# Kernel tuning notes

Measured on AMD Instinct MI355X. Metric: run time of the kernel, lower is better.

The kernel has to match this reference:

```python
import jax, jax.numpy as jnp
import numpy as np

TWO_PI = 2.0 * np.pi


def _grid_sample(w, g):
    """Bilinear sample. w: [M,C,H,W]; g: [M,2,H,W] coords in [-1,1] (x,y),
    align_corners=True, border-clamped."""
    H, W = w.shape[-2], w.shape[-1]
    x = (g[:, 0] + 1.0) * 0.5 * (W - 1)  # [M,H,W]
    y = (g[:, 1] + 1.0) * 0.5 * (H - 1)
    x0 = jnp.floor(x)
    y0 = jnp.floor(y)
    fx = x - x0
    fy = y - y0
    x0i = jnp.clip(x0.astype(jnp.int32), 0, W - 1)
    x1i = jnp.clip(x0i + 1, 0, W - 1)
    y0i = jnp.clip(y0.astype(jnp.int32), 0, H - 1)
    y1i = jnp.clip(y0i + 1, 0, H - 1)

    def samp(wm, yi, xi):
        return wm[:, yi, xi]  # [C,H,W]

    v00 = jax.vmap(samp)(w, y0i, x0i)
    v01 = jax.vmap(samp)(w, y0i, x1i)
    v10 = jax.vmap(samp)(w, y1i, x0i)
    v11 = jax.vmap(samp)(w, y1i, x1i)
    fx = fx[:, None]  # broadcast over channel dim
    fy = fy[:, None]
    return (1 - fy) * ((1 - fx) * v00 + fx * v01) + fy * ((1 - fx) * v10 + fx * v11)


def _forward(in_H, out_H, weight, grid_H, grid_Rn, mask):
    No, Ni = out_H.shape[0], in_H.shape[0]
    N = grid_H.shape[0]
    Gk, Cout, Cin, kh, kw = weight.shape

    # inverse_H: angles negate; left_apply_to_H: angles add (pairwise)
    out_inv = -out_H  # [No,1]
    theta = (out_inv[:, None, 0] + in_H[None, :, 0]).reshape(-1)  # [No*Ni]

    # interpolate_H: periodic linear interp over uniform angle grid
    step = TWO_PI / N
    pos = jnp.mod(theta, TWO_PI) / step
    i0 = jnp.floor(pos).astype(jnp.int32) % N
    i1 = (i0 + 1) % N
    frac = (pos - jnp.floor(pos))[:, None]
    wflat = weight.reshape(Gk, -1)  # [Gk, Cout*Cin*kh*kw]
    w = (1.0 - frac) * wflat[i0] + frac * wflat[i1]  # [No*Ni, C]
    w = w.reshape(No * Ni, Cin * Cout, kh, kw)

    # left_apply_to_Rn: rotate spatial grid by out_H^{-1}
    ang = out_inv[:, 0]
    c, s = jnp.cos(ang), jnp.sin(ang)
    gx = c[:, None, None] * grid_Rn[0] - s[:, None, None] * grid_Rn[1]
    gy = s[:, None, None] * grid_Rn[0] + c[:, None, None] * grid_Rn[1]
    grids = jnp.stack([gx, gy], axis=1)  # [No,2,kh,kw]
    grids = jnp.repeat(grids, Ni, axis=0)  # repeat_interleave -> [No*Ni,2,kh,kw]

    # interpolate_Rn: bilinear grid sample
    w = _grid_sample(w, grids)  # [No*Ni, Cin*Cout, kh, kw]
    w = w.reshape(No, Ni, Cin, Cout, kh, kw)
    # .transpose(0,3).transpose(1,3) -> [Cout, No, Cin, Ni, kh, kw]
    w = jnp.transpose(w, (3, 0, 2, 1, 4, 5))
    return mask * w


def setup_inputs() -> dict:
    key = jax.random.key(0)
    k1, k2, k3 = jax.random.split(key, 3)
    N, Cout, Cin, ks = 8, 128, 128, 5
    in_H = jax.random.uniform(k1, (N, 1), dtype=jnp.float32) * TWO_PI
    out_H = jax.random.uniform(k2, (N, 1), dtype=jnp.float32) * TWO_PI
    fan_in = Cin * ks * ks
    weight = jax.random.normal(k3, (N, Cout, Cin, ks, ks), dtype=jnp.float32) / np.sqrt(fan_in)
    grid_H = (jnp.arange(N) * (TWO_PI / N)).astype(jnp.float32)
    lin = jnp.linspace(-1.0, 1.0, ks)
    X, Y = jnp.meshgrid(lin, lin, indexing='xy')
    grid_Rn = jnp.stack([X, Y]).astype(jnp.float32)  # [2, ks, ks]
    mask = (X ** 2 + Y ** 2 <= 1.0 + 1e-6).astype(jnp.float32)  # circular mask
    return dict(in_H=in_H, out_H=out_H, weight=weight, grid_H=grid_H,
                grid_Rn=grid_Rn, mask=mask)


def reference(in_H, out_H, weight, grid_H, grid_Rn, mask):
    return _forward(in_H, out_H, weight, grid_H, grid_Rn, mask)
```

## Files before the change

kernel.cpp:

```cpp
#include <hip/hip_runtime.h>
#include <math.h>


#define TWO_PI_F 6.28318530717958647692f
#define G_STRIDE 808

__global__ __launch_bounds__(256) void rotconv_weight_kernel(
    const float* __restrict__ in_H,
    const float* __restrict__ out_H,
    const float* __restrict__ weight,
    const float* __restrict__ grid_Rn,
    const float* __restrict__ mask,
    float* __restrict__ out)
{
    __shared__ __align__(16) float s_w[8 * G_STRIDE];

    const int t  = threadIdx.x;
    const int bx = blockIdx.x;
    const int vt = bx & 63;
    const int ut = (bx >> 6) & 7;
    const int o  = bx >> 9;
    const int u0 = ut * 16;
    const int v0 = vt * 2;

    for (int j = t; j < 3200; j += 256) {
        const int chunk = j / 25;
        const int off   = j - chunk * 25;
        const int g = chunk >> 4;
        const int u = chunk & 15;
        const float2 w2 = *reinterpret_cast<const float2*>(
            weight + ((size_t)((g * 128 + u0 + u) * 128) + v0) * 25 + (size_t)off * 2);
        *reinterpret_cast<float2*>(s_w + g * G_STRIDE + u * 50 + off * 2) = w2;
    }

    const int ii = t / 25;
    const int k  = t - ii * 25;
    const bool active = (t < 200);
    const int i = ii > 7 ? 7 : ii;

    const float ang = -out_H[o];

    const float theta = in_H[i] + ang;
    float m = fmodf(theta, TWO_PI_F);
    if (m < 0.0f) m += TWO_PI_F;
    const float pos  = m * (8.0f / TWO_PI_F);
    const float pf   = floorf(pos);
    const float frac = pos - pf;
    const int g0 = ((int)pf) & 7;
    const int g1 = (g0 + 1) & 7;
    const float om = 1.0f - frac;

    float sthe, cthe;
    sincosf(ang, &sthe, &cthe);
    const float X = grid_Rn[k];
    const float Y = grid_Rn[25 + k];
    const float gx = cthe * X - sthe * Y;
    const float gy = sthe * X + cthe * Y;
    const float x = (gx + 1.0f) * 2.0f;
    const float y = (gy + 1.0f) * 2.0f;
    const float x0f = floorf(x);
    const float y0f = floorf(y);
    const float fx = x - x0f;
    const float fy = y - y0f;
    int x0 = (int)x0f; x0 = x0 < 0 ? 0 : (x0 > 4 ? 4 : x0);
    int y0 = (int)y0f; y0 = y0 < 0 ? 0 : (y0 > 4 ? 4 : y0);
    const int y1 = y0 + 1 > 4 ? 4 : y0 + 1;
    const float mk = mask[k];
    float wa = mk * (1.0f - fy) * (1.0f - fx);
    float wb = mk * (1.0f - fy) * fx;
    float wc = mk * fy * (1.0f - fx);
    float wd = mk * fy * fx;
    int xb = x0;
    if (x0 == 4) { xb = 3; wb += wa; wa = 0.0f; wd += wc; wc = 0.0f; }
    const int rb0 = y0 * 5 + xb;
    const int rb1 = y1 * 5 + xb;
    const float a00 = om * wa,  a01 = om * wb,  a10 = om * wc,  a11 = om * wd;
    const float b00 = frac * wa, b01 = frac * wb, b10 = frac * wc, b11 = frac * wd;

    __syncthreads();

    if (!active) return;

    const float* tg0 = s_w + g0 * G_STRIDE;
    const float* tg1 = s_w + g1 * G_STRIDE;
    const size_t ob0 = (((size_t)v0 * 8 + o) * 128 + u0) * 200 + t;
    const size_t ob1 = ((((size_t)v0 + 1) * 8 + o) * 128 + u0) * 200 + t;

#pragma unroll
    for (int uu = 0; uu < 16; ++uu) {
#pragma unroll
        for (int vv = 0; vv < 2; ++vv) {
            const int run = uu * 2 + vv;
            const float* p0 = tg0 + run * 25;
            const float* p1 = tg1 + run * 25;
            const float v00 = p0[rb0], v01 = p0[rb0 + 1];
            const float v10 = p0[rb1], v11 = p0[rb1 + 1];
            const float w00 = p1[rb0], w01 = p1[rb0 + 1];
            const float w10 = p1[rb1], w11 = p1[rb1 + 1];
            const float val = a00 * v00 + a01 * v01 + a10 * v10 + a11 * v11
                            + b00 * w00 + b01 * w01 + b10 * w10 + b11 * w11;
            out[(vv ? ob1 : ob0) + (size_t)uu * 200] = val;
        }
    }
}

extern "C" void kernel_launch(void* const* d_in, const int* in_sizes, int n_in,
                              void* d_out, int out_size, void* d_ws, size_t ws_size,
                              hipStream_t stream) {
    const float* in_H    = (const float*)d_in[0];
    const float* out_H   = (const float*)d_in[1];
    const float* weight  = (const float*)d_in[2];
    const float* grid_Rn = (const float*)d_in[4];
    const float* mask    = (const float*)d_in[5];
    float* out = (float*)d_out;

    rotconv_weight_kernel<<<dim3(4096), dim3(256), 0, stream>>>(
        in_H, out_H, weight, grid_Rn, mask, out);
}
```

Measured before the change: 149.4 us.

## Pre-blend angular interpolation into shared memory per input angle

Each input angle's two-group angular interpolation is now done once while loading the weight tile into shared memory, storing 8 blended tiles instead of 8 raw group tiles. The sampling stage then reads 4 shared values per output instead of 8. Threads whose mask is zero skip the shared reads, the output stores are grouped in chunks of 8, and the launch bounds now ask for 6 blocks per SM. The load phase now does two global reads per element (with cache reuse across angles) plus an extra barrier for the per-angle coefficients.

```diff
diff --git a/kernel.cpp b/kernel.cpp
--- a/kernel.cpp
+++ b/kernel.cpp
@@ -3,9 +3,9 @@
 
 
 #define TWO_PI_F 6.28318530717958647692f
-#define G_STRIDE 808
+#define T_STRIDE 812
 
-__global__ __launch_bounds__(256) void rotconv_weight_kernel(
+__global__ __launch_bounds__(256, 6) void rotconv_weight_kernel(
     const float* __restrict__ in_H,
     const float* __restrict__ out_H,
     const float* __restrict__ weight,
@@ -13,7 +13,9 @@
     const float* __restrict__ mask,
     float* __restrict__ out)
 {
-    __shared__ __align__(16) float s_w[8 * G_STRIDE];
+    __shared__ __align__(16) float s_w[8 * T_STRIDE];
+    __shared__ float s_fr[8];
+    __shared__ int   s_g0[8], s_g1[8];
 
     const int t  = threadIdx.x;
     const int bx = blockIdx.x;
@@ -23,32 +25,40 @@
     const int u0 = ut * 16;
     const int v0 = vt * 2;
 
+    const float ang = -out_H[o];
+
+    if (t < 8) {
+        const float theta = in_H[t] + ang;
+        float m = fmodf(theta, TWO_PI_F);
+        if (m < 0.0f) m += TWO_PI_F;
+        const float pos = m * (8.0f / TWO_PI_F);
+        const float pf  = floorf(pos);
+        s_fr[t] = pos - pf;
+        const int g0 = ((int)pf) & 7;
+        s_g0[t] = g0;
+        s_g1[t] = (g0 + 1) & 7;
+    }
+    __syncthreads();
+
     for (int j = t; j < 3200; j += 256) {
-        const int chunk = j / 25;
-        const int off   = j - chunk * 25;
-        const int g = chunk >> 4;
-        const int u = chunk & 15;
-        const float2 w2 = *reinterpret_cast<const float2*>(
-            weight + ((size_t)((g * 128 + u0 + u) * 128) + v0) * 25 + (size_t)off * 2);
-        *reinterpret_cast<float2*>(s_w + g * G_STRIDE + u * 50 + off * 2) = w2;
+        const int i2 = j / 400;
+        const int r  = j - i2 * 400;
+        const int u  = r / 25;
+        const int e  = r - u * 25;
+        const int g0 = s_g0[i2], g1 = s_g1[i2];
+        const float fr = s_fr[i2], om = 1.0f - fr;
+        const size_t sbase = ((size_t)((u0 + u) * 128) + v0) * 25 + (size_t)e * 2;
+        const float2 a = *reinterpret_cast<const float2*>(weight + (size_t)g0 * 409600 + sbase);
+        const float2 b = *reinterpret_cast<const float2*>(weight + (size_t)g1 * 409600 + sbase);
+        float2 bl;
+        bl.x = om * a.x + fr * b.x;
+        bl.y = om * a.y + fr * b.y;
+        *reinterpret_cast<float2*>(s_w + i2 * T_STRIDE + u * 50 + e * 2) = bl;
     }
 
     const int ii = t / 25;
     const int k  = t - ii * 25;
-    const bool active = (t < 200);
-    const int i = ii > 7 ? 7 : ii;
-
-    const float ang = -out_H[o];
-
-    const float theta = in_H[i] + ang;
-    float m = fmodf(theta, TWO_PI_F);
-    if (m < 0.0f) m += TWO_PI_F;
-    const float pos  = m * (8.0f / TWO_PI_F);
-    const float pf   = floorf(pos);
-    const float frac = pos - pf;
-    const int g0 = ((int)pf) & 7;
-    const int g1 = (g0 + 1) & 7;
-    const float om = 1.0f - frac;
+    const int i  = ii > 7 ? 7 : ii;
 
     float sthe, cthe;
     sincosf(ang, &sthe, &cthe);
@@ -74,32 +84,33 @@
     if (x0 == 4) { xb = 3; wb += wa; wa = 0.0f; wd += wc; wc = 0.0f; }
     const int rb0 = y0 * 5 + xb;
     const int rb1 = y1 * 5 + xb;
-    const float a00 = om * wa,  a01 = om * wb,  a10 = om * wc,  a11 = om * wd;
-    const float b00 = frac * wa, b01 = frac * wb, b10 = frac * wc, b11 = frac * wd;
+    const bool has = (mk != 0.0f);
 
     __syncthreads();
 
-    if (!active) return;
+    if (t >= 200) return;
 
-    const float* tg0 = s_w + g0 * G_STRIDE;
-    const float* tg1 = s_w + g1 * G_STRIDE;
+    const float* sm = s_w + i * T_STRIDE;
     const size_t ob0 = (((size_t)v0 * 8 + o) * 128 + u0) * 200 + t;
-    const size_t ob1 = ((((size_t)v0 + 1) * 8 + o) * 128 + u0) * 200 + t;
+    const size_t ob1 = ob0 + 204800;
 
+    for (int c = 0; c < 4; ++c) {
+        float vals[8];
 #pragma unroll
-    for (int uu = 0; uu < 16; ++uu) {
+        for (int r8 = 0; r8 < 8; ++r8) vals[r8] = 0.0f;
+        if (has) {
 #pragma unroll
-        for (int vv = 0; vv < 2; ++vv) {
-            const int run = uu * 2 + vv;
-            const float* p0 = tg0 + run * 25;
-            const float* p1 = tg1 + run * 25;
-            const float v00 = p0[rb0], v01 = p0[rb0 + 1];
-            const float v10 = p0[rb1], v11 = p0[rb1 + 1];
-            const float w00 = p1[rb0], w01 = p1[rb0 + 1];
-            const float w10 = p1[rb1], w11 = p1[rb1 + 1];
-            const float val = a00 * v00 + a01 * v01 + a10 * v10 + a11 * v11
-                            + b00 * w00 + b01 * w01 + b10 * w10 + b11 * w11;
-            out[(vv ? ob1 : ob0) + (size_t)uu * 200] = val;
+            for (int r8 = 0; r8 < 8; ++r8) {
+                const float* tp = sm + (c * 8 + r8) * 25;
+                vals[r8] = wa * tp[rb0] + wb * tp[rb0 + 1]
+                         + wc * tp[rb1] + wd * tp[rb1 + 1];
+            }
+        }
+#pragma unroll
+        for (int r8 = 0; r8 < 8; ++r8) {
+            const int run = c * 8 + r8;
+            const int uu  = run >> 1;
+            out[((run & 1) ? ob1 : ob0) + (size_t)uu * 200] = vals[r8];
         }
     }
 }
```

After: 145.6 us. -2.6%, faster.
